# Optimization experiments

Measured on AMD Instinct MI355X. Metric: run time of the kernel, lower is better.

Reference implementation:

```python
import jax, jax.numpy as jnp
import numpy as np

H = 1024          # hidden_size
M = 512           # moe_intermediate_size
E = 16            # n_routed_experts
TOP_K = 4         # num_experts_per_tok
N_GROUP = 4
TOPK_GROUP = 2
SCALE = 2.5       # routed_scaling_factor
B, S = 2, 1024


def setup_inputs() -> dict:
    key = jax.random.key(0)
    ks = jax.random.split(key, 9)
    sc_h = 1.0 / np.sqrt(H)
    sc_m = 1.0 / np.sqrt(M)
    return {
        "hidden_states": jax.random.normal(ks[0], (B, S, H), jnp.float32),
        "gate_kernel": jax.random.normal(ks[1], (H, E), jnp.float32) * sc_h,
        "gate_bias": jax.random.normal(ks[2], (E,), jnp.float32) * 0.01,
        "w_gate": jax.random.normal(ks[3], (E, H, M), jnp.float32) * sc_h,
        "w_up": jax.random.normal(ks[4], (E, H, M), jnp.float32) * sc_h,
        "w_down": jax.random.normal(ks[5], (E, M, H), jnp.float32) * sc_m,
        "sw_gate": jax.random.normal(ks[6], (H, 2 * M), jnp.float32) * sc_h,
        "sw_up": jax.random.normal(ks[7], (H, 2 * M), jnp.float32) * sc_h,
        "sw_down": jax.random.normal(ks[8], (2 * M, H), jnp.float32) * (1.0 / np.sqrt(2 * M)),
    }


def _gate(x2d, gate_kernel, gate_bias):
    # x2d: [N, H]
    n = x2d.shape[0]
    logits = jnp.dot(x2d.astype(jnp.float32), gate_kernel.astype(jnp.float32))  # [N, E]
    scores = jax.nn.sigmoid(logits)
    scores_for_choice = scores + gate_bias  # noaux_tc correction bias
    # group-limited top-k: sum of top-2 scores per group
    group_scores = scores_for_choice.reshape(n, N_GROUP, E // N_GROUP)
    top2 = jax.lax.top_k(group_scores, k=2)[0]
    group_sum = jnp.sum(top2, axis=-1)                       # [N, G]
    group_idx = jax.lax.top_k(group_sum, k=TOPK_GROUP)[1]    # [N, topk_group]
    group_mask = jnp.zeros_like(group_sum).at[jnp.arange(n)[:, None], group_idx].set(1.0)
    score_mask = jnp.repeat(group_mask[:, :, None], E // N_GROUP, axis=2).reshape(n, E)
    masked_scores = jnp.where(score_mask > 0, scores_for_choice, 0.0)
    topk_weight, topk_idx = jax.lax.top_k(masked_scores, k=TOP_K)
    # norm_topk_prob
    topk_weight = topk_weight / (jnp.sum(topk_weight, axis=-1, keepdims=True) + 1e-20)
    topk_weight = topk_weight * SCALE
    return topk_idx, topk_weight


def reference(hidden_states, gate_kernel, gate_bias, w_gate, w_up, w_down,
              sw_gate, sw_up, sw_down):
    orig_shape = hidden_states.shape
    x = hidden_states.reshape(-1, orig_shape[-1])  # [N, H]
    topk_idx, topk_weight = _gate(x, gate_kernel, gate_bias)
    # combine weight per (token, expert): sum_k (topk_idx==e) * topk_weight
    onehot = (topk_idx[:, :, None] == jnp.arange(E)[None, None, :]).astype(topk_weight.dtype)
    combine = jnp.einsum('nke,nk->ne', onehot, topk_weight)  # [N, E]
    # dense per-expert MLP (faithful to moe_infer which runs every expert)
    g = jnp.einsum('nh,ehm->enm', x, w_gate)   # [E, N, M]
    u = jnp.einsum('nh,ehm->enm', x, w_up)
    inter = jax.nn.silu(g) * u
    y_e = jnp.einsum('enm,emh->enh', inter, w_down)          # [E, N, H]
    y = jnp.einsum('ne,enh->nh', combine, y_e)               # [N, H]
    # shared-expert path
    shared = jnp.dot(jax.nn.silu(jnp.dot(x, sw_gate)) * jnp.dot(x, sw_up), sw_down)
    return (y + shared).reshape(orig_shape)
```

## Files before the change

kernel.cpp:

```cpp
#include <hip/hip_runtime.h>
#include <hip/hip_bf16.h>
#include <cstdint>

#define HID    1024
#define MID    512
#define NEXP   16
#define NTOKS  2048
#define TOPKE  4
#define RSCALE 2.5f
#define CSTR   16

typedef __attribute__((ext_vector_type(8))) short  bf16x8;
typedef __attribute__((ext_vector_type(8))) ushort u16x8;
typedef __attribute__((ext_vector_type(4))) float  f32x4;

__device__ __forceinline__ ushort f2bf(float f){
  unsigned u = __float_as_uint(f);
  u += 0x7fffu + ((u >> 16) & 1u);
  return (ushort)(u >> 16);
}
__device__ __forceinline__ float bf2f(ushort h){ return __uint_as_float(((unsigned)h) << 16); }

#define GLD16(g, l) __builtin_amdgcn_global_load_lds( \
    (const __attribute__((address_space(1))) unsigned int*)(g), \
    (__attribute__((address_space(3))) unsigned int*)(l), 16, 0, 0)

__device__ __forceinline__ void tr_tile(const float* __restrict__ in,
                                        ushort* __restrict__ out,
                                        int K, int N, int kb, int nb,
                                        float* __restrict__ T)
{
  const int t  = threadIdx.x;
  const int r  = t >> 4;
  const int c4 = (t & 15) * 4;
  #pragma unroll
  for (int i = 0; i < 4; ++i){
    f32x4 v = *reinterpret_cast<const f32x4*>(in + (size_t)(kb + r + i*16) * N + nb + c4);
    #pragma unroll
    for (int j = 0; j < 4; ++j)
      T[(r + i*16) * 65 + c4 + j] = v[j];
  }
  __syncthreads();
  const int n = t >> 2;
  const int q = t & 3;
  u16x8 o0, o1;
  #pragma unroll
  for (int j = 0; j < 8; ++j) o0[j] = f2bf(T[(q*16 + j) * 65 + n]);
  #pragma unroll
  for (int j = 0; j < 8; ++j) o1[j] = f2bf(T[(q*16 + 8 + j) * 65 + n]);
  ushort* op = out + (size_t)(nb + n) * K + kb + q * 16;
  *reinterpret_cast<u16x8*>(op)     = o0;
  *reinterpret_cast<u16x8*>(op + 8) = o1;
}

__global__ __launch_bounds__(256) void k_pre0(
    const float* __restrict__ x, ushort* __restrict__ xb,
    const float* __restrict__ gk, const float* __restrict__ gb,
    const float* __restrict__ swg, const float* __restrict__ swu,
    const float* __restrict__ swd,
    ushort* __restrict__ swgT, ushort* __restrict__ swuT,
    ushort* __restrict__ swdT,
    int* __restrict__ counts, int* __restrict__ tidx, float* __restrict__ tw)
{
  __shared__ float T[64 * 65];
  __shared__ float sc[16][16];
  __shared__ int lcnt[NEXP];
  const int z = blockIdx.z;
  const int bid = blockIdx.y * 8 + blockIdx.x;

  if (z < 6){
    const int m = z >> 1;
    const float* in = (m == 0) ? swg : (m == 1) ? swu : swd;
    ushort* out     = (m == 0) ? swgT : (m == 1) ? swuT : swdT;
    tr_tile(in, out, 1024, 1024, blockIdx.y * 64, (z & 1) * 512 + blockIdx.x * 64, T);
    return;
  }
  if (z == 6){
    #pragma unroll
    for (int j = 0; j < 8; ++j){
      int i = bid * 2048 + j * 256 + threadIdx.x;
      f32x4 a = *reinterpret_cast<const f32x4*>(x + (size_t)i*8);
      f32x4 b = *reinterpret_cast<const f32x4*>(x + (size_t)i*8 + 4);
      u16x8 o;
      o[0]=f2bf(a[0]); o[1]=f2bf(a[1]); o[2]=f2bf(a[2]); o[3]=f2bf(a[3]);
      o[4]=f2bf(b[0]); o[5]=f2bf(b[1]); o[6]=f2bf(b[2]); o[7]=f2bf(b[3]);
      *reinterpret_cast<u16x8*>(xb + (size_t)i*8) = o;
    }
    return;
  }
  {
    const int tid = threadIdx.x;
    const int tl  = tid >> 4;
    const int e   = tid & 15;
    const int t   = bid * 16 + tl;
    float acc = 0.f;
    const float* xr = x + (size_t)t * HID;
    for (int h = 0; h < HID; h += 4){
      f32x4 xv = *reinterpret_cast<const f32x4*>(xr + h);
      acc += xv[0] * gk[(h+0)*NEXP + e];
      acc += xv[1] * gk[(h+1)*NEXP + e];
      acc += xv[2] * gk[(h+2)*NEXP + e];
      acc += xv[3] * gk[(h+3)*NEXP + e];
    }
    sc[tl][e] = 1.f / (1.f + expf(-acc)) + gb[e];
    if (tid < NEXP) lcnt[tid] = 0;
    __syncthreads();
    if (tid < 16){
      const int tt = bid * 16 + tid;
      float s4[NEXP];
      #pragma unroll
      for (int i = 0; i < NEXP; ++i) s4[i] = sc[tid][i];
      float gs[4];
      #pragma unroll
      for (int g = 0; g < 4; ++g){
        float m1 = -1e30f, m2 = -1e30f;
        #pragma unroll
        for (int j = 0; j < 4; ++j){
          float v = s4[g*4+j];
          if (v > m1){ m2 = m1; m1 = v; } else if (v > m2){ m2 = v; }
        }
        gs[g] = m1 + m2;
      }
      int g1 = 0;
      for (int g = 1; g < 4; ++g) if (gs[g] > gs[g1]) g1 = g;
      int g2 = -1;
      for (int g = 0; g < 4; ++g){
        if (g == g1) continue;
        if (g2 < 0 || gs[g] > gs[g2]) g2 = g;
      }
      float ms[NEXP];
      #pragma unroll
      for (int i = 0; i < NEXP; ++i){
        int g = i >> 2;
        ms[i] = (g == g1 || g == g2) ? s4[i] : 0.0f;
      }
      bool used[NEXP];
      #pragma unroll
      for (int i = 0; i < NEXP; ++i) used[i] = false;
      int sel[TOPKE]; float val[TOPKE]; float denom = 0.f;
      #pragma unroll
      for (int k = 0; k < TOPKE; ++k){
        int be = -1; float bv = -1e30f;
        for (int i = 0; i < NEXP; ++i){
          if (used[i]) continue;
          if (ms[i] > bv){ bv = ms[i]; be = i; }
        }
        used[be] = true; sel[k] = be; val[k] = bv; denom += bv;
      }
      float inv = RSCALE / (denom + 1e-20f);
      #pragma unroll
      for (int k = 0; k < TOPKE; ++k){
        tidx[tt*TOPKE + k] = sel[k];
        tw  [tt*TOPKE + k] = val[k] * inv;
        atomicAdd(&lcnt[sel[k]], 1);
      }
    }
    __syncthreads();
    if (tid < NEXP && lcnt[tid]) atomicAdd(&counts[tid * CSTR], lcnt[tid]);
  }
}

__global__ __launch_bounds__(256) void k_place(const int* __restrict__ tidx,
                                               const float* __restrict__ tw,
                                               const int* __restrict__ counts,
                                               int* __restrict__ cursor,
                                               int* __restrict__ tlist,
                                               float* __restrict__ wlist,
                                               int* __restrict__ pos)
{
  __shared__ int lcnt[NEXP];
  __shared__ int lbase[NEXP];
  __shared__ int soff[NEXP];
  const int tid = threadIdx.x;
  const int t = blockIdx.x * 256 + tid;
  if (tid < NEXP){
    lcnt[tid] = 0;
    int s = 0;
    for (int i = 0; i < tid; ++i) s += counts[i * CSTR];
    soff[tid] = s;
  }
  __syncthreads();
  int sel[TOPKE]; float w4[TOPKE]; int ls[TOPKE];
  #pragma unroll
  for (int k = 0; k < TOPKE; ++k){
    sel[k] = tidx[t*TOPKE + k];
    w4[k]  = tw[t*TOPKE + k];
    ls[k]  = atomicAdd(&lcnt[sel[k]], 1);
  }
  __syncthreads();
  if (tid < NEXP) lbase[tid] = atomicAdd(&cursor[tid * CSTR], lcnt[tid]);
  __syncthreads();
  #pragma unroll
  for (int k = 0; k < TOPKE; ++k){
    int p = soff[sel[k]] + lbase[sel[k]] + ls[k];
    tlist[p] = t;
    wlist[p] = w4[k];
    pos[t*TOPKE + k] = p;
  }
}

__global__ __launch_bounds__(256) void k_mmS(
    const ushort* __restrict__ xb, ushort* __restrict__ i_s,
    const ushort* __restrict__ swgT, const ushort* __restrict__ swuT,
    const float* __restrict__ wg, const float* __restrict__ wu,
    ushort* __restrict__ wgT, ushort* __restrict__ wuT)
{
  __shared__ __align__(16) ushort Sh[16384];
  const int z = blockIdx.z;
  if (z >= 2){
    const bool isU = (z >= 18);
    const int e = isU ? (z - 18) : (z - 2);
    const float* in = (isU ? wu : wg) + (size_t)e * HID * MID;
    ushort* out     = (isU ? wuT : wgT) + (size_t)e * HID * MID;
    tr_tile(in, out, 1024, 512, blockIdx.y * 64, blockIdx.x * 64, (float*)Sh);
    return;
  }

  const int mbase   = blockIdx.y * 128;
  const int colBase = z * 512 + blockIdx.x * 64;

  const int tid = threadIdx.x;
  const int l   = tid & 63;
  const int w   = tid >> 6;
  const int wm  = w >> 1;
  const int wn  = w & 1;

  const int rl     = l >> 3;
  const int srcOff = 8 * ((l & 7) ^ rl);

  const ushort* srcP[8];
  #pragma unroll
  for (int j = 0; j < 8; ++j){
    int g = w * 8 + j;
    const ushort* p;
    if (g < 16){
      p = xb + (size_t)(mbase + g * 8 + rl) * HID;
    } else if (g < 24){
      p = swgT + (size_t)(colBase + (g - 16) * 8 + rl) * HID;
    } else {
      p = swuT + (size_t)(colBase + (g - 24) * 8 + rl) * HID;
    }
    srcP[j] = p + srcOff;
  }

  f32x4 accg[4][2], accu[4][2];
  #pragma unroll
  for (int i = 0; i < 4; ++i)
    #pragma unroll
    for (int j = 0; j < 2; ++j){
      accg[i][j] = (f32x4){0.f,0.f,0.f,0.f};
      accu[i][j] = (f32x4){0.f,0.f,0.f,0.f};
    }

  const int fr  = l & 15;
  const int ko  = l >> 4;
  const int swz = (fr & 7) << 4;

  for (int kt = 0; kt < 16; ++kt){
    const int ke = kt * 64;
    #pragma unroll
    for (int j = 0; j < 8; ++j)
      GLD16(srcP[j] + ke, (ushort*)Sh + (w*8 + j) * 512 + l * 8);
    __syncthreads();
    #pragma unroll
    for (int ks = 0; ks < 2; ++ks){
      const int co = ks * 64 + ko * 16;
      bf16x8 af[4], bg[2], bu[2];
      #pragma unroll
      for (int mf = 0; mf < 4; ++mf)
        af[mf] = *reinterpret_cast<const bf16x8*>(
            (const char*)Sh + (wm*64 + mf*16 + fr) * 128 + (co ^ swz));
      #pragma unroll
      for (int nf = 0; nf < 2; ++nf){
        int cc = wn*32 + nf*16 + fr;
        bg[nf] = *reinterpret_cast<const bf16x8*>(
            (const char*)Sh + 16384 + cc * 128 + (co ^ swz));
        bu[nf] = *reinterpret_cast<const bf16x8*>(
            (const char*)Sh + 24576 + cc * 128 + (co ^ swz));
      }
      #pragma unroll
      for (int mf = 0; mf < 4; ++mf)
        #pragma unroll
        for (int nf = 0; nf < 2; ++nf){
          accg[mf][nf] = __builtin_amdgcn_mfma_f32_16x16x32_bf16(af[mf], bg[nf], accg[mf][nf], 0, 0, 0);
          accu[mf][nf] = __builtin_amdgcn_mfma_f32_16x16x32_bf16(af[mf], bu[nf], accu[mf][nf], 0, 0, 0);
        }
    }
    __syncthreads();
  }

  const int ccol = l & 15;
  const int crow = (l >> 4) * 4;
  #pragma unroll
  for (int mf = 0; mf < 4; ++mf){
    #pragma unroll
    for (int r_ = 0; r_ < 4; ++r_){
      const int row = wm*64 + mf*16 + crow + r_ + mbase;
      #pragma unroll
      for (int nf = 0; nf < 2; ++nf){
        int col = colBase + wn*32 + nf*16 + ccol;
        float g = accg[mf][nf][r_];
        float u = accu[mf][nf][r_];
        float s = g / (1.f + expf(-g));
        i_s[(size_t)row * 1024 + col] = f2bf(s * u);
      }
    }
  }
}

__global__ __launch_bounds__(256) void k_mmR(
    const ushort* __restrict__ xb, ushort* __restrict__ i_r,
    const ushort* __restrict__ wgT, const ushort* __restrict__ wuT,
    const float* __restrict__ wd, ushort* __restrict__ wdT,
    const int* __restrict__ counts, const int* __restrict__ tlist)
{
  __shared__ __align__(16) ushort Sh[16384];
  const int z = blockIdx.z;
  if (z >= 16){
    const int e = z - 16;
    tr_tile(wd + (size_t)e * MID * HID, wdT + (size_t)e * MID * HID,
            512, 1024, blockIdx.x * 64, blockIdx.y * 64, (float*)Sh);
    return;
  }

  const int e = z;
  const int mbase = blockIdx.y * 128;
  const int cnt = counts[e * CSTR];
  if (mbase >= cnt) return;
  int aoff = 0;
  for (int i = 0; i < e; ++i) aoff += counts[i * CSTR];

  const int colBase = blockIdx.x * 64;
  const ushort* Bg = wgT + (size_t)e * MID * HID;
  const ushort* Bu = wuT + (size_t)e * MID * HID;

  const int tid = threadIdx.x;
  const int l   = tid & 63;
  const int w   = tid >> 6;
  const int wm  = w >> 1;
  const int wn  = w & 1;

  const int rl     = l >> 3;
  const int srcOff = 8 * ((l & 7) ^ rl);

  const ushort* srcP[8];
  #pragma unroll
  for (int j = 0; j < 8; ++j){
    int g = w * 8 + j;
    const ushort* p;
    if (g < 16){
      int ar = mbase + g * 8 + rl;
      int s = aoff + (ar < cnt ? ar : cnt - 1);
      p = xb + (size_t)tlist[s] * HID;
    } else if (g < 24){
      p = Bg + (size_t)(colBase + (g - 16) * 8 + rl) * HID;
    } else {
      p = Bu + (size_t)(colBase + (g - 24) * 8 + rl) * HID;
    }
    srcP[j] = p + srcOff;
  }

  f32x4 accg[4][2], accu[4][2];
  #pragma unroll
  for (int i = 0; i < 4; ++i)
    #pragma unroll
    for (int j = 0; j < 2; ++j){
      accg[i][j] = (f32x4){0.f,0.f,0.f,0.f};
      accu[i][j] = (f32x4){0.f,0.f,0.f,0.f};
    }

  const int fr  = l & 15;
  const int ko  = l >> 4;
  const int swz = (fr & 7) << 4;

  for (int kt = 0; kt < 16; ++kt){
    const int ke = kt * 64;
    #pragma unroll
    for (int j = 0; j < 8; ++j)
      GLD16(srcP[j] + ke, (ushort*)Sh + (w*8 + j) * 512 + l * 8);
    __syncthreads();
    #pragma unroll
    for (int ks = 0; ks < 2; ++ks){
      const int co = ks * 64 + ko * 16;
      bf16x8 af[4], bg[2], bu[2];
      #pragma unroll
      for (int mf = 0; mf < 4; ++mf)
        af[mf] = *reinterpret_cast<const bf16x8*>(
            (const char*)Sh + (wm*64 + mf*16 + fr) * 128 + (co ^ swz));
      #pragma unroll
      for (int nf = 0; nf < 2; ++nf){
        int cc = wn*32 + nf*16 + fr;
        bg[nf] = *reinterpret_cast<const bf16x8*>(
            (const char*)Sh + 16384 + cc * 128 + (co ^ swz));
        bu[nf] = *reinterpret_cast<const bf16x8*>(
            (const char*)Sh + 24576 + cc * 128 + (co ^ swz));
      }
      #pragma unroll
      for (int mf = 0; mf < 4; ++mf)
        #pragma unroll
        for (int nf = 0; nf < 2; ++nf){
          accg[mf][nf] = __builtin_amdgcn_mfma_f32_16x16x32_bf16(af[mf], bg[nf], accg[mf][nf], 0, 0, 0);
          accu[mf][nf] = __builtin_amdgcn_mfma_f32_16x16x32_bf16(af[mf], bu[nf], accu[mf][nf], 0, 0, 0);
        }
    }
    __syncthreads();
  }

  const int ccol = l & 15;
  const int crow = (l >> 4) * 4;
  #pragma unroll
  for (int mf = 0; mf < 4; ++mf){
    #pragma unroll
    for (int r_ = 0; r_ < 4; ++r_){
      const int arel = wm*64 + mf*16 + crow + r_ + mbase;
      if (arel >= cnt) continue;
      size_t row = (size_t)(aoff + arel);
      #pragma unroll
      for (int nf = 0; nf < 2; ++nf){
        int col = colBase + wn*32 + nf*16 + ccol;
        float g = accg[mf][nf][r_];
        float u = accu[mf][nf][r_];
        float s = g / (1.f + expf(-g));
        i_r[row * 512 + col] = f2bf(s * u);
      }
    }
  }
}

__global__ __launch_bounds__(256) void k_mm1(
    const ushort* __restrict__ i_s, const ushort* __restrict__ i_r,
    const ushort* __restrict__ swdT, const ushort* __restrict__ wdT,
    ushort* __restrict__ y_s, ushort* __restrict__ y_r,
    const int* __restrict__ counts, const float* __restrict__ wlist)
{
  const int z = blockIdx.z;
  const bool routed = (z > 0);
  const int e = z - 1;
  const int Kd = routed ? MID : HID;
  const int mbase = blockIdx.y * 128;
  const int nbase = blockIdx.x * 128;
  int cnt = NTOKS, aoff = 0;
  if (routed){
    cnt = counts[e * CSTR];
    if (mbase >= cnt) return;
    for (int i = 0; i < e; ++i) aoff += counts[i * CSTR];
  }
  const ushort* A = routed ? i_r : i_s;
  const ushort* B = routed ? (wdT + (size_t)e * HID * MID) : swdT;

  __shared__ __align__(16) ushort Sh[16384];

  const int tid = threadIdx.x;
  const int l   = tid & 63;
  const int w   = tid >> 6;
  const int wm  = w >> 1;
  const int wn  = w & 1;

  const int rl     = l >> 3;
  const int srcOff = 8 * ((l & 7) ^ rl);

  const ushort* srcP[8];
  #pragma unroll
  for (int j = 0; j < 8; ++j){
    int g = w * 8 + j;
    const ushort* p;
    if (g < 16){
      int ar = mbase + g * 8 + rl;
      if (routed){
        int s = aoff + (ar < cnt ? ar : cnt - 1);
        p = A + (size_t)s * Kd;
      } else p = A + (size_t)ar * Kd;
    } else {
      p = B + (size_t)(nbase + (g - 16) * 8 + rl) * Kd;
    }
    srcP[j] = p + srcOff;
  }

  f32x4 acc[4][4];
  #pragma unroll
  for (int i = 0; i < 4; ++i)
    #pragma unroll
    for (int j = 0; j < 4; ++j)
      acc[i][j] = (f32x4){0.f,0.f,0.f,0.f};

  const int fr  = l & 15;
  const int ko  = l >> 4;
  const int swz = (fr & 7) << 4;
  const int nk  = Kd >> 6;

  for (int kt = 0; kt < nk; ++kt){
    const int ke = kt * 64;
    #pragma unroll
    for (int j = 0; j < 8; ++j)
      GLD16(srcP[j] + ke, (ushort*)Sh + (w*8 + j) * 512 + l * 8);
    __syncthreads();
    #pragma unroll
    for (int ks = 0; ks < 2; ++ks){
      const int co = ks * 64 + ko * 16;
      bf16x8 af[4], bf[4];
      #pragma unroll
      for (int mf = 0; mf < 4; ++mf)
        af[mf] = *reinterpret_cast<const bf16x8*>(
            (const char*)Sh + (wm*64 + mf*16 + fr) * 128 + (co ^ swz));
      #pragma unroll
      for (int nf = 0; nf < 4; ++nf)
        bf[nf] = *reinterpret_cast<const bf16x8*>(
            (const char*)Sh + 16384 + (wn*64 + nf*16 + fr) * 128 + (co ^ swz));
      #pragma unroll
      for (int mf = 0; mf < 4; ++mf)
        #pragma unroll
        for (int nf = 0; nf < 4; ++nf)
          acc[mf][nf] = __builtin_amdgcn_mfma_f32_16x16x32_bf16(af[mf], bf[nf], acc[mf][nf], 0, 0, 0);
    }
    __syncthreads();
  }

  const int ccol = l & 15;
  const int crow = (l >> 4) * 4;
  #pragma unroll
  for (int mf = 0; mf < 4; ++mf){
    #pragma unroll
    for (int r_ = 0; r_ < 4; ++r_){
      const int arel = wm*64 + mf*16 + crow + r_ + mbase;
      if (routed && arel >= cnt) continue;
      if (!routed){
        #pragma unroll
        for (int nf = 0; nf < 4; ++nf){
          int col = nbase + wn*64 + nf*16 + ccol;
          y_s[(size_t)arel * HID + col] = f2bf(acc[mf][nf][r_]);
        }
      } else {
        int s = aoff + arel;
        float wgt = wlist[s];
        #pragma unroll
        for (int nf = 0; nf < 4; ++nf){
          int col = nbase + wn*64 + nf*16 + ccol;
          y_r[(size_t)s * HID + col] = f2bf(wgt * acc[mf][nf][r_]);
        }
      }
    }
  }
}

__global__ __launch_bounds__(256) void k_comb(const ushort* __restrict__ y_s,
                                              const ushort* __restrict__ y_r,
                                              const int* __restrict__ pos,
                                              float* __restrict__ out)
{
  const int t  = blockIdx.x * 2 + (threadIdx.x >> 7);
  const int c8 = (threadIdx.x & 127) * 8;
  const int* pp = pos + t * TOPKE;
  u16x8 vs = *reinterpret_cast<const u16x8*>(y_s + (size_t)t * HID + c8);
  float s[8];
  #pragma unroll
  for (int j = 0; j < 8; ++j) s[j] = bf2f(vs[j]);
  #pragma unroll
  for (int k = 0; k < TOPKE; ++k){
    int p = pp[k];
    u16x8 vr = *reinterpret_cast<const u16x8*>(y_r + (size_t)p * HID + c8);
    #pragma unroll
    for (int j = 0; j < 8; ++j) s[j] += bf2f(vr[j]);
  }
  f32x4 o0 = (f32x4){s[0],s[1],s[2],s[3]};
  f32x4 o1 = (f32x4){s[4],s[5],s[6],s[7]};
  *reinterpret_cast<f32x4*>(out + (size_t)t * HID + c8)     = o0;
  *reinterpret_cast<f32x4*>(out + (size_t)t * HID + c8 + 4) = o1;
}

extern "C" void kernel_launch(void* const* d_in, const int* in_sizes, int n_in,
                              void* d_out, int out_size, void* d_ws, size_t ws_size,
                              hipStream_t stream)
{
  const float* x   = (const float*)d_in[0];
  const float* gk  = (const float*)d_in[1];
  const float* gb  = (const float*)d_in[2];
  const float* wg  = (const float*)d_in[3];
  const float* wu  = (const float*)d_in[4];
  const float* wd  = (const float*)d_in[5];
  const float* swg = (const float*)d_in[6];
  const float* swu = (const float*)d_in[7];
  const float* swd = (const float*)d_in[8];
  float* out = (float*)d_out;
  char* ws = (char*)d_ws;

  const size_t MB = 1ull << 20;
  int*    counts = (int*)(ws + 0);
  int*    cursor = (int*)(ws + 2048);
  int*    tidx   = (int*)(ws + 8192);
  float*  tw     = (float*)(ws + 49152);
  int*    tlist  = (int*)(ws + 90112);
  float*  wlist  = (float*)(ws + 131072);
  int*    pos    = (int*)(ws + 163840);
  ushort* xb     = (ushort*)(ws + 1*MB);
  ushort* swgT   = (ushort*)(ws + 5*MB);
  ushort* swuT   = (ushort*)(ws + 7*MB);
  ushort* swdT   = (ushort*)(ws + 9*MB);
  ushort* wgT    = (ushort*)(ws + 11*MB);
  ushort* wuT    = (ushort*)(ws + 27*MB);
  ushort* wdT    = (ushort*)(ws + 43*MB);
  ushort* i_s    = (ushort*)(ws + 59*MB);
  ushort* i_r    = (ushort*)(ws + 63*MB);
  ushort* y_r    = (ushort*)(ws + 11*MB);
  ushort* y_s    = (ushort*)(ws + 27*MB);

  hipMemsetAsync(ws, 0, 4096, stream);
  k_pre0<<<dim3(8,16,8), 256, 0, stream>>>(x, xb, gk, gb, swg, swu, swd,
                                           swgT, swuT, swdT, counts, tidx, tw);
  k_place<<<NTOKS/256, 256, 0, stream>>>(tidx, tw, counts, cursor, tlist, wlist, pos);

  k_mmS<<<dim3(8,16,34), 256, 0, stream>>>(xb, i_s, swgT, swuT, wg, wu, wgT, wuT);
  k_mmR<<<dim3(8,16,32), 256, 0, stream>>>(xb, i_r, wgT, wuT, wd, wdT, counts, tlist);
  k_mm1<<<dim3(8,16,17), 256, 0, stream>>>(i_s, i_r, swdT, wdT, y_s, y_r,
                                           counts, wlist);
  k_comb<<<NTOKS/2, 256, 0, stream>>>(y_s, y_r, pos, out);
}
```

Measured before the change: 163.9 us.

## Rebalance stage work: move wd transpose earlier and shared down-proj into routed-up kernel

The w_down transpose tiles move from the routed gate/up kernel into the earlier shared gate/up kernel. The shared-expert down projection moves from the final GEMM kernel into the routed gate/up launch as an extra z-slice. Each launch now holds a more even mix of independent work, which is meant to cut tail imbalance and improve CU fill. y_s gets its own workspace region so it no longer aliases wuT, which is still read concurrently. The cost is a heavier first kernel and an extra 4MB of workspace.

```diff
diff --git a/kernel.cpp b/kernel.cpp
--- a/kernel.cpp
+++ b/kernel.cpp
@@ -203,10 +203,18 @@
     const ushort* __restrict__ xb, ushort* __restrict__ i_s,
     const ushort* __restrict__ swgT, const ushort* __restrict__ swuT,
     const float* __restrict__ wg, const float* __restrict__ wu,
-    ushort* __restrict__ wgT, ushort* __restrict__ wuT)
+    const float* __restrict__ wd,
+    ushort* __restrict__ wgT, ushort* __restrict__ wuT,
+    ushort* __restrict__ wdT)
 {
   __shared__ __align__(16) ushort Sh[16384];
   const int z = blockIdx.z;
+  if (z >= 34){
+    const int e = z - 34;
+    tr_tile(wd + (size_t)e * MID * HID, wdT + (size_t)e * MID * HID,
+            512, 1024, blockIdx.x * 64, blockIdx.y * 64, (float*)Sh);
+    return;
+  }
   if (z >= 2){
     const bool isU = (z >= 18);
     const int e = isU ? (z - 18) : (z - 2);
@@ -311,15 +319,81 @@
 __global__ __launch_bounds__(256) void k_mmR(
     const ushort* __restrict__ xb, ushort* __restrict__ i_r,
     const ushort* __restrict__ wgT, const ushort* __restrict__ wuT,
-    const float* __restrict__ wd, ushort* __restrict__ wdT,
+    const ushort* __restrict__ i_s, const ushort* __restrict__ swdT,
+    ushort* __restrict__ y_s,
     const int* __restrict__ counts, const int* __restrict__ tlist)
 {
   __shared__ __align__(16) ushort Sh[16384];
   const int z = blockIdx.z;
-  if (z >= 16){
-    const int e = z - 16;
-    tr_tile(wd + (size_t)e * MID * HID, wdT + (size_t)e * MID * HID,
-            512, 1024, blockIdx.x * 64, blockIdx.y * 64, (float*)Sh);
+
+  const int tid = threadIdx.x;
+  const int l   = tid & 63;
+  const int w   = tid >> 6;
+  const int wm  = w >> 1;
+  const int wn  = w & 1;
+  const int rl     = l >> 3;
+  const int srcOff = 8 * ((l & 7) ^ rl);
+  const int fr  = l & 15;
+  const int ko  = l >> 4;
+  const int swz = (fr & 7) << 4;
+  const int ccol = l & 15;
+  const int crow = (l >> 4) * 4;
+
+  if (z == 16){
+    const int mbase = blockIdx.y * 128;
+    const int nbase = blockIdx.x * 128;
+    const ushort* srcP[8];
+    #pragma unroll
+    for (int j = 0; j < 8; ++j){
+      int g = w * 8 + j;
+      const ushort* p;
+      if (g < 16) p = i_s + (size_t)(mbase + g * 8 + rl) * HID;
+      else        p = swdT + (size_t)(nbase + (g - 16) * 8 + rl) * HID;
+      srcP[j] = p + srcOff;
+    }
+    f32x4 acc[4][4];
+    #pragma unroll
+    for (int i = 0; i < 4; ++i)
+      #pragma unroll
+      for (int j = 0; j < 4; ++j)
+        acc[i][j] = (f32x4){0.f,0.f,0.f,0.f};
+    for (int kt = 0; kt < 16; ++kt){
+      const int ke = kt * 64;
+      #pragma unroll
+      for (int j = 0; j < 8; ++j)
+        GLD16(srcP[j] + ke, (ushort*)Sh + (w*8 + j) * 512 + l * 8);
+      __syncthreads();
+      #pragma unroll
+      for (int ks = 0; ks < 2; ++ks){
+        const int co = ks * 64 + ko * 16;
+        bf16x8 af[4], bf[4];
+        #pragma unroll
+        for (int mf = 0; mf < 4; ++mf)
+          af[mf] = *reinterpret_cast<const bf16x8*>(
+              (const char*)Sh + (wm*64 + mf*16 + fr) * 128 + (co ^ swz));
+        #pragma unroll
+        for (int nf = 0; nf < 4; ++nf)
+          bf[nf] = *reinterpret_cast<const bf16x8*>(
+              (const char*)Sh + 16384 + (wn*64 + nf*16 + fr) * 128 + (co ^ swz));
+        #pragma unroll
+        for (int mf = 0; mf < 4; ++mf)
+          #pragma unroll
+          for (int nf = 0; nf < 4; ++nf)
+            acc[mf][nf] = __builtin_amdgcn_mfma_f32_16x16x32_bf16(af[mf], bf[nf], acc[mf][nf], 0, 0, 0);
+      }
+      __syncthreads();
+    }
+    #pragma unroll
+    for (int mf = 0; mf < 4; ++mf)
+      #pragma unroll
+      for (int r_ = 0; r_ < 4; ++r_){
+        const int row = wm*64 + mf*16 + crow + r_ + mbase;
+        #pragma unroll
+        for (int nf = 0; nf < 4; ++nf){
+          int col = nbase + wn*64 + nf*16 + ccol;
+          y_s[(size_t)row * HID + col] = f2bf(acc[mf][nf][r_]);
+        }
+      }
     return;
   }
 
@@ -333,15 +407,6 @@
   const int colBase = blockIdx.x * 64;
   const ushort* Bg = wgT + (size_t)e * MID * HID;
   const ushort* Bu = wuT + (size_t)e * MID * HID;
-
-  const int tid = threadIdx.x;
-  const int l   = tid & 63;
-  const int w   = tid >> 6;
-  const int wm  = w >> 1;
-  const int wn  = w & 1;
-
-  const int rl     = l >> 3;
-  const int srcOff = 8 * ((l & 7) ^ rl);
 
   const ushort* srcP[8];
   #pragma unroll
@@ -369,10 +434,6 @@
       accu[i][j] = (f32x4){0.f,0.f,0.f,0.f};
     }
 
-  const int fr  = l & 15;
-  const int ko  = l >> 4;
-  const int swz = (fr & 7) << 4;
-
   for (int kt = 0; kt < 16; ++kt){
     const int ke = kt * 64;
     #pragma unroll
@@ -406,8 +467,6 @@
     __syncthreads();
   }
 
-  const int ccol = l & 15;
-  const int crow = (l >> 4) * 4;
   #pragma unroll
   for (int mf = 0; mf < 4; ++mf){
     #pragma unroll
@@ -428,25 +487,18 @@
 }
 
 __global__ __launch_bounds__(256) void k_mm1(
-    const ushort* __restrict__ i_s, const ushort* __restrict__ i_r,
-    const ushort* __restrict__ swdT, const ushort* __restrict__ wdT,
-    ushort* __restrict__ y_s, ushort* __restrict__ y_r,
+    const ushort* __restrict__ i_r, const ushort* __restrict__ wdT,
+    ushort* __restrict__ y_r,
     const int* __restrict__ counts, const float* __restrict__ wlist)
 {
-  const int z = blockIdx.z;
-  const bool routed = (z > 0);
-  const int e = z - 1;
-  const int Kd = routed ? MID : HID;
+  const int e = blockIdx.z;
   const int mbase = blockIdx.y * 128;
   const int nbase = blockIdx.x * 128;
-  int cnt = NTOKS, aoff = 0;
-  if (routed){
-    cnt = counts[e * CSTR];
-    if (mbase >= cnt) return;
-    for (int i = 0; i < e; ++i) aoff += counts[i * CSTR];
-  }
-  const ushort* A = routed ? i_r : i_s;
-  const ushort* B = routed ? (wdT + (size_t)e * HID * MID) : swdT;
+  const int cnt = counts[e * CSTR];
+  if (mbase >= cnt) return;
+  int aoff = 0;
+  for (int i = 0; i < e; ++i) aoff += counts[i * CSTR];
+  const ushort* B = wdT + (size_t)e * HID * MID;
 
   __shared__ __align__(16) ushort Sh[16384];
 
@@ -455,7 +507,6 @@
   const int w   = tid >> 6;
   const int wm  = w >> 1;
   const int wn  = w & 1;
-
   const int rl     = l >> 3;
   const int srcOff = 8 * ((l & 7) ^ rl);
 
@@ -466,12 +517,10 @@
     const ushort* p;
     if (g < 16){
       int ar = mbase + g * 8 + rl;
-      if (routed){
-        int s = aoff + (ar < cnt ? ar : cnt - 1);
-        p = A + (size_t)s * Kd;
-      } else p = A + (size_t)ar * Kd;
+      int s = aoff + (ar < cnt ? ar : cnt - 1);
+      p = i_r + (size_t)s * MID;
     } else {
-      p = B + (size_t)(nbase + (g - 16) * 8 + rl) * Kd;
+      p = B + (size_t)(nbase + (g - 16) * 8 + rl) * MID;
     }
     srcP[j] = p + srcOff;
   }
@@ -486,9 +535,8 @@
   const int fr  = l & 15;
   const int ko  = l >> 4;
   const int swz = (fr & 7) << 4;
-  const int nk  = Kd >> 6;
-
-  for (int kt = 0; kt < nk; ++kt){
+
+  for (int kt = 0; kt < 8; ++kt){
     const int ke = kt * 64;
     #pragma unroll
     for (int j = 0; j < 8; ++j)
@@ -522,21 +570,13 @@
     #pragma unroll
     for (int r_ = 0; r_ < 4; ++r_){
       const int arel = wm*64 + mf*16 + crow + r_ + mbase;
-      if (routed && arel >= cnt) continue;
-      if (!routed){
-        #pragma unroll
-        for (int nf = 0; nf < 4; ++nf){
-          int col = nbase + wn*64 + nf*16 + ccol;
-          y_s[(size_t)arel * HID + col] = f2bf(acc[mf][nf][r_]);
-        }
-      } else {
-        int s = aoff + arel;
-        float wgt = wlist[s];
-        #pragma unroll
-        for (int nf = 0; nf < 4; ++nf){
-          int col = nbase + wn*64 + nf*16 + ccol;
-          y_r[(size_t)s * HID + col] = f2bf(wgt * acc[mf][nf][r_]);
-        }
+      if (arel >= cnt) continue;
+      int s = aoff + arel;
+      float wgt = wlist[s];
+      #pragma unroll
+      for (int nf = 0; nf < 4; ++nf){
+        int col = nbase + wn*64 + nf*16 + ccol;
+        y_r[(size_t)s * HID + col] = f2bf(wgt * acc[mf][nf][r_]);
       }
     }
   }
@@ -600,17 +640,18 @@
   ushort* wdT    = (ushort*)(ws + 43*MB);
   ushort* i_s    = (ushort*)(ws + 59*MB);
   ushort* i_r    = (ushort*)(ws + 63*MB);
+  ushort* y_s    = (ushort*)(ws + 71*MB);
   ushort* y_r    = (ushort*)(ws + 11*MB);
-  ushort* y_s    = (ushort*)(ws + 27*MB);
 
   hipMemsetAsync(ws, 0, 4096, stream);
   k_pre0<<<dim3(8,16,8), 256, 0, stream>>>(x, xb, gk, gb, swg, swu, swd,
                                            swgT, swuT, swdT, counts, tidx, tw);
   k_place<<<NTOKS/256, 256, 0, stream>>>(tidx, tw, counts, cursor, tlist, wlist, pos);
 
-  k_mmS<<<dim3(8,16,34), 256, 0, stream>>>(xb, i_s, swgT, swuT, wg, wu, wgT, wuT);
-  k_mmR<<<dim3(8,16,32), 256, 0, stream>>>(xb, i_r, wgT, wuT, wd, wdT, counts, tlist);
-  k_mm1<<<dim3(8,16,17), 256, 0, stream>>>(i_s, i_r, swdT, wdT, y_s, y_r,
-                                           counts, wlist);
+  k_mmS<<<dim3(8,16,50), 256, 0, stream>>>(xb, i_s, swgT, swuT, wg, wu, wd,
+                                           wgT, wuT, wdT);
+  k_mmR<<<dim3(8,16,17), 256, 0, stream>>>(xb, i_r, wgT, wuT, i_s, swdT, y_s,
+                                           counts, tlist);
+  k_mm1<<<dim3(8,16,16), 256, 0, stream>>>(i_r, wdT, y_r, counts, wlist);
   k_comb<<<NTOKS/2, 256, 0, stream>>>(y_s, y_r, pos, out);
 }
```

Measured after the change: 165.1 us (median of 2 runs). No clear change (+0.7%).
